# Kernel optimization log

Measured on AMD Instinct MI355X. Metric: run time of the kernel, lower is better.

The kernel has to match this reference:

```python
import jax, jax.numpy as jnp
import numpy as np

N_NODES = 100000
N_EDGES = 1600000
IN_DIM = 128
OUT_DIM = 128


def setup_inputs() -> dict:
    key = jax.random.key(0)
    ks = jax.random.split(key, 8)
    x = jax.random.normal(ks[0], (N_NODES, IN_DIM), dtype=jnp.float32)
    one_hot_h = jax.random.normal(ks[1], (N_NODES, OUT_DIM), dtype=jnp.float32)
    # three candidate-op linear transforms (in_dim -> out_dim)
    W0 = jax.random.normal(ks[2], (IN_DIM, OUT_DIM), dtype=jnp.float32) * 0.05
    W1 = jax.random.normal(ks[3], (IN_DIM, OUT_DIM), dtype=jnp.float32) * 0.05
    W2 = jax.random.normal(ks[4], (IN_DIM, OUT_DIM), dtype=jnp.float32) * 0.05
    # sparse mask_matrix in COO form: out[r] += v * H[c]
    mask_rows = jax.random.randint(ks[5], (N_EDGES,), 0, N_NODES, dtype=jnp.int32)
    mask_cols = jax.random.randint(ks[6], (N_EDGES,), 0, N_NODES, dtype=jnp.int32)
    mask_vals = jax.random.uniform(ks[7], (N_EDGES,), dtype=jnp.float32)
    return {"x": x, "one_hot_h": one_hot_h, "W0": W0, "W1": W1, "W2": W2,
            "mask_rows": mask_rows, "mask_cols": mask_cols, "mask_vals": mask_vals}


def reference(x, one_hot_h, W0, W1, W2, mask_rows, mask_cols, mask_vals):
    # Original: sum_k spmm(mask_matrix, op_k(x)) + spmm(mask_matrix, one_hot_h).
    # spmm is linear, so summing per-op outputs pre-aggregation is exact and
    # fuses K spmm launches into one sparse aggregation pass.
    H = x @ W0 + x @ W1 + x @ W2 + one_hot_h              # [N, out_dim]
    gathered = mask_vals[:, None] * H[mask_cols]          # [E, out_dim]
    out = jax.ops.segment_sum(gathered, mask_rows, num_segments=x.shape[0])
    return out
```

## Files before the change

### kernel.cpp

```cpp
#include <hip/hip_runtime.h>
#include <hip/hip_bf16.h>

#define N_NODES 100000
#define N_EDGES 1600000
#define DIM 128

#define NBIN 512
#define RPP  196
#define PCAP 4096
#define P1_BLOCKS 512
#define CHUNK (N_EDGES / P1_BLOCKS)

typedef unsigned int uint_t;
typedef unsigned short ushort_t;
typedef float f32x4 __attribute__((ext_vector_type(4)));
typedef __bf16 bf16x8 __attribute__((ext_vector_type(8)));

__device__ inline uint_t f2bf(float f) {
    uint_t u = __float_as_uint(f);
    return (u + 0x7FFFu + ((u >> 16) & 1u)) >> 16;
}
__device__ inline float bf2f(uint_t lo16) { return __uint_as_float(lo16 << 16); }

__global__ __launch_bounds__(256) void pass1_bin(
        const int* __restrict__ rows, const int* __restrict__ cols,
        const float* __restrict__ vals, int* __restrict__ psize,
        long long* __restrict__ slab,
        const float* __restrict__ W0, const float* __restrict__ W1,
        const float* __restrict__ W2, ushort_t* __restrict__ WT) {
    if (blockIdx.x >= P1_BLOCKS) {
        int i = (blockIdx.x - P1_BLOCKS) * 256 + threadIdx.x;
        if (i < DIM * DIM) {
            int m = i & 127, k = i >> 7;
            float s = W0[k * DIM + m] + W1[k * DIM + m] + W2[k * DIM + m];
            WT[m * DIM + k] = (ushort_t)f2bf(s);
        }
        return;
    }
    __shared__ int hist[NBIN];
    __shared__ int binoff[NBIN];
    __shared__ int resv[NBIN];
    __shared__ int curs[NBIN];
    __shared__ long long ebuf[CHUNK];
    __shared__ int edest[CHUNK];

    int t = threadIdx.x;
    int e0 = blockIdx.x * CHUNK;

    for (int i = t; i < NBIN; i += 256) hist[i] = 0;
    __syncthreads();

    for (int i = t; i < CHUNK; i += 256) {
        int r = rows[e0 + i];
        atomicAdd(&hist[r / RPP], 1);
    }
    __syncthreads();

    if (t < 64) {
        int b = t * 8;
        int v[8]; int s = 0;
#pragma unroll
        for (int k = 0; k < 8; ++k) { v[k] = hist[b + k]; s += v[k]; }
        int incl = s;
#pragma unroll
        for (int d = 1; d < 64; d <<= 1) {
            int o = __shfl_up(incl, d, 64);
            if (t >= d) incl += o;
        }
        int run = incl - s;
#pragma unroll
        for (int k = 0; k < 8; ++k) { binoff[b + k] = run; run += v[k]; }
    }
    __syncthreads();

    for (int i = t; i < NBIN; i += 256) {
        int len = hist[i];
        int r = (len > 0) ? atomicAdd(&psize[i], len) : 0;
        resv[i] = i * PCAP + r;
        curs[i] = binoff[i];
    }
    __syncthreads();

    for (int i = t; i < CHUNK; i += 256) {
        int   r = rows[e0 + i];
        int   c = cols[e0 + i];
        float v = vals[e0 + i];
        int b  = r / RPP;
        int lr = r - b * RPP;
        int pos = atomicAdd(&curs[b], 1);
        uint_t key = ((uint_t)lr << 17) | (uint_t)c;
        ebuf[pos]  = ((long long)__float_as_int(v) << 32) | (long long)key;
        edest[pos] = resv[b] + (pos - binoff[b]);
    }
    __syncthreads();

    for (int i = t; i < CHUNK; i += 256)
        slab[edest[i]] = ebuf[i];
}

__global__ __launch_bounds__(256) void pass2_sort(
        const long long* __restrict__ slab, const int* __restrict__ psize,
        int* __restrict__ off, long long* __restrict__ csr) {
    __shared__ int pb[NBIN + 1];
    __shared__ int cnt[RPP + 1];
    __shared__ int loff[RPP + 1];
    __shared__ int curs[RPP];
    __shared__ long long ebuf[PCAP];

    int p = blockIdx.x, t = threadIdx.x;

    if (t < 64) {
        int b = t * 8;
        int v[8]; int s = 0;
#pragma unroll
        for (int k = 0; k < 8; ++k) { v[k] = min(psize[b + k], PCAP); s += v[k]; }
        int incl = s;
#pragma unroll
        for (int d = 1; d < 64; d <<= 1) {
            int o = __shfl_up(incl, d, 64);
            if (t >= d) incl += o;
        }
        int run = incl - s;
#pragma unroll
        for (int k = 0; k < 8; ++k) { pb[b + k] = run; run += v[k]; }
        if (t == 63) pb[NBIN] = incl;
    }
    for (int i = t; i < RPP + 1; i += 256) cnt[i] = 0;
    __syncthreads();

    int n = min(psize[p], PCAP);
    int base = pb[p];
    int rlo = p * RPP;
    int nrows = N_NODES - rlo;
    if (nrows > RPP) nrows = RPP;
    if (nrows < 0) nrows = 0;
    const long long* seg = slab + (long long)p * PCAP;

    if (p == NBIN - 1 && t == 0) off[N_NODES] = pb[NBIN];

    for (int i = t; i < n; i += 256) {
        long long ev = __builtin_nontemporal_load(&seg[i]);
        ebuf[i] = ev;
        uint_t key = (uint_t)(ev & 0xFFFFFFFFll);
        atomicAdd(&cnt[key >> 17], 1);
    }
    __syncthreads();

    if (t < 64) {
        int b4 = t * 4;
        int v[4]; int s = 0;
#pragma unroll
        for (int k = 0; k < 4; ++k) {
            int idx = b4 + k;
            v[k] = (idx < RPP) ? cnt[idx] : 0;
            s += v[k];
        }
        int incl = s;
#pragma unroll
        for (int d = 1; d < 64; d <<= 1) {
            int o = __shfl_up(incl, d, 64);
            if (t >= d) incl += o;
        }
        int run = incl - s;
#pragma unroll
        for (int k = 0; k < 4; ++k) {
            int idx = b4 + k;
            if (idx < RPP) loff[idx] = run;
            run += v[k];
        }
    }
    __syncthreads();

    for (int i = t; i < nrows; i += 256) {
        curs[i] = loff[i];
        off[rlo + i] = base + loff[i];
    }
    __syncthreads();

    for (int i = t; i < n; i += 256) {
        long long ev = ebuf[i];
        uint_t key = (uint_t)(ev & 0xFFFFFFFFll);
        int lr = key >> 17;
        uint_t c = key & 0x1FFFFu;
        int pos = atomicAdd(&curs[lr], 1);
        csr[base + pos] = (long long)(((unsigned long long)ev & 0xFFFFFFFF00000000ull) | c);
    }
}

#define GROWS 64
#define XSTR 136
__global__ __launch_bounds__(256) void gemm_mfma(const float* __restrict__ x,
                                                 const float* __restrict__ oh,
                                                 const ushort_t* __restrict__ WT,
                                                 uint_t* __restrict__ H16) {
    __shared__ ushort_t xs[GROWS * XSTR];
    int tid = threadIdx.x;
    int wv = tid >> 6, l = tid & 63;
    int lr = l & 15, kg = l >> 4;
    int lrow = wv * 16 + lr;
    long long base_row = (long long)blockIdx.x * GROWS;
    long long hr = base_row + lrow;

    const f32x4* xg = (const f32x4*)x;
#pragma unroll
    for (int i = 0; i < 8; ++i) {
        int g = tid + i * 256;
        int row = g >> 5, c4 = g & 31;
        long long sr = base_row + row; if (sr >= N_NODES) sr = N_NODES - 1;
        f32x4 v = __builtin_nontemporal_load(xg + sr * 32 + c4);
        ushort_t* d = &xs[row * XSTR + c4 * 4];
        d[0] = (ushort_t)f2bf(v.x); d[1] = (ushort_t)f2bf(v.y);
        d[2] = (ushort_t)f2bf(v.z); d[3] = (ushort_t)f2bf(v.w);
    }
    __syncthreads();

    f32x4 acc[8] = {};
#pragma unroll
    for (int s = 0; s < 4; ++s) {
        bf16x8 b = *(const bf16x8*)&xs[lrow * XSTR + s * 32 + kg * 8];
#pragma unroll
        for (int mt = 0; mt < 8; ++mt) {
            bf16x8 a = *(const bf16x8*)&WT[(mt * 16 + lr) * DIM + s * 32 + kg * 8];
            acc[mt] = __builtin_amdgcn_mfma_f32_16x16x32_bf16(a, b, acc[mt], 0, 0, 0);
        }
    }
    __syncthreads();

    const f32x4* og = (const f32x4*)oh;
#pragma unroll
    for (int i = 0; i < 8; ++i) {
        int g = tid + i * 256;
        int row = g >> 5, c4 = g & 31;
        long long sr = base_row + row; if (sr >= N_NODES) sr = N_NODES - 1;
        f32x4 v = __builtin_nontemporal_load(og + sr * 32 + c4);
        ushort_t* d = &xs[row * XSTR + c4 * 4];
        d[0] = (ushort_t)f2bf(v.x); d[1] = (ushort_t)f2bf(v.y);
        d[2] = (ushort_t)f2bf(v.z); d[3] = (ushort_t)f2bf(v.w);
    }
    __syncthreads();

    if (hr < N_NODES) {
#pragma unroll
        for (int mt = 0; mt < 8; ++mt) {
            int c0 = mt * 16 + kg * 4;
            const uint_t* ow = (const uint_t*)&xs[lrow * XSTR + c0];
            uint_t w0 = ow[0], w1 = ow[1];
            float f0 = acc[mt].x + bf2f(w0 & 0xFFFFu);
            float f1 = acc[mt].y + bf2f(w0 >> 16);
            float f2 = acc[mt].z + bf2f(w1 & 0xFFFFu);
            float f3 = acc[mt].w + bf2f(w1 >> 16);
            uint2 pk;
            pk.x = f2bf(f0) | (f2bf(f1) << 16);
            pk.y = f2bf(f2) | (f2bf(f3) << 16);
            *(uint2*)&H16[(size_t)hr * (DIM / 2) + c0 / 2] = pk;
        }
    }
}

__global__ __launch_bounds__(256) void gather_kernel(const uint_t* __restrict__ H16,
                                                     const int* __restrict__ off,
                                                     const long long* __restrict__ csr,
                                                     float* __restrict__ out) {
    int tid  = threadIdx.x;
    int wave = tid >> 6;
    int lane = tid & 63;
    int grp  = lane >> 4;
    int il   = lane & 15;
    int wid  = blockIdx.x * 16 + wave * 4 + grp;

    int s = off[wid], e = off[wid + 1];
    float acc[8] = {};

#define ACC8(h, v)                                                            \
    acc[0] += (v) * bf2f((h).x & 0xFFFFu); acc[1] += (v) * bf2f((h).x >> 16); \
    acc[2] += (v) * bf2f((h).y & 0xFFFFu); acc[3] += (v) * bf2f((h).y >> 16); \
    acc[4] += (v) * bf2f((h).z & 0xFFFFu); acc[5] += (v) * bf2f((h).z >> 16); \
    acc[6] += (v) * bf2f((h).w & 0xFFFFu); acc[7] += (v) * bf2f((h).w >> 16);

    int p = s;
    for (; p + 3 < e; p += 4) {
        long long cv0 = __builtin_nontemporal_load(&csr[p]);
        long long cv1 = __builtin_nontemporal_load(&csr[p + 1]);
        long long cv2 = __builtin_nontemporal_load(&csr[p + 2]);
        long long cv3 = __builtin_nontemporal_load(&csr[p + 3]);
        uint4 h0 = *(const uint4*)&H16[(long long)(int)(cv0 & 0x1FFFF) * (DIM / 2) + il * 4];
        uint4 h1 = *(const uint4*)&H16[(long long)(int)(cv1 & 0x1FFFF) * (DIM / 2) + il * 4];
        uint4 h2 = *(const uint4*)&H16[(long long)(int)(cv2 & 0x1FFFF) * (DIM / 2) + il * 4];
        uint4 h3 = *(const uint4*)&H16[(long long)(int)(cv3 & 0x1FFFF) * (DIM / 2) + il * 4];
        float v0 = __int_as_float((int)(cv0 >> 32));
        float v1 = __int_as_float((int)(cv1 >> 32));
        float v2 = __int_as_float((int)(cv2 >> 32));
        float v3 = __int_as_float((int)(cv3 >> 32));
        ACC8(h0, v0) ACC8(h1, v1) ACC8(h2, v2) ACC8(h3, v3)
    }
    for (; p < e; ++p) {
        long long cv = __builtin_nontemporal_load(&csr[p]);
        float v = __int_as_float((int)(cv >> 32));
        uint4 h = *(const uint4*)&H16[(long long)(int)(cv & 0x1FFFF) * (DIM / 2) + il * 4];
        ACC8(h, v)
    }
#undef ACC8

    float* op = &out[(long long)wid * DIM + il * 8];
    f32x4 o0 = {acc[0], acc[1], acc[2], acc[3]};
    f32x4 o1 = {acc[4], acc[5], acc[6], acc[7]};
    __builtin_nontemporal_store(o0, (f32x4*)op);
    __builtin_nontemporal_store(o1, (f32x4*)(op + 4));
}

extern "C" void kernel_launch(void* const* d_in, const int* in_sizes, int n_in,
                              void* d_out, int out_size, void* d_ws, size_t ws_size,
                              hipStream_t stream) {
    const float* x    = (const float*)d_in[0];
    const float* oh   = (const float*)d_in[1];
    const float* W0   = (const float*)d_in[2];
    const float* W1   = (const float*)d_in[3];
    const float* W2   = (const float*)d_in[4];
    const int*   rows = (const int*)d_in[5];
    const int*   cols = (const int*)d_in[6];
    const float* vals = (const float*)d_in[7];
    float* out = (float*)d_out;

    char* p = (char*)d_ws;
    size_t oW    = 0;
    size_t oH    = oW + 64 * 1024;
    size_t oOff  = oH + (size_t)N_NODES * DIM * 2;
    size_t oPs   = oOff + (size_t)(N_NODES + 32) * 4;
    size_t oSlab = oPs + 4096;
    size_t oCsr  = oSlab + (size_t)NBIN * PCAP * 8;

    ushort_t*  WT    = (ushort_t*)(p + oW);
    uint_t*    H16   = (uint_t*)(p + oH);
    int*       off   = (int*)(p + oOff);
    int*       psize = (int*)(p + oPs);
    long long* slab  = (long long*)(p + oSlab);
    long long* csr   = (long long*)(p + oCsr);

    (void)hipMemsetAsync(psize, 0, NBIN * sizeof(int), stream);
    pass1_bin<<<P1_BLOCKS + 64, 256, 0, stream>>>(rows, cols, vals, psize, slab,
                                                  W0, W1, W2, WT);
    pass2_sort<<<NBIN, 256, 0, stream>>>(slab, psize, off, csr);
    gemm_mfma<<<(N_NODES + GROWS - 1) / GROWS, 256, 0, stream>>>(x, oh, WT, H16);
    gather_kernel<<<N_NODES / 16, 256, 0, stream>>>(H16, off, csr, out);
}
```

Before: 161.9 us.

## Fuse edge binning pass with dense GEMM into one interleaved launch

```diff
diff --git a/kernel.cpp b/kernel.cpp
--- a/kernel.cpp
+++ b/kernel.cpp
@@ -10,6 +10,7 @@
 #define PCAP 4096
 #define P1_BLOCKS 512
 #define CHUNK (N_EDGES / P1_BLOCKS)
+#define GEMM_BLOCKS 1563
 
 typedef unsigned int uint_t;
 typedef unsigned short ushort_t;
@@ -22,80 +23,166 @@
 }
 __device__ inline float bf2f(uint_t lo16) { return __uint_as_float(lo16 << 16); }
 
-__global__ __launch_bounds__(256) void pass1_bin(
+__global__ __launch_bounds__(256) void wt_init(const float* __restrict__ W0,
+                                               const float* __restrict__ W1,
+                                               const float* __restrict__ W2,
+                                               ushort_t* __restrict__ WT,
+                                               int* __restrict__ psize) {
+    if (blockIdx.x == 64) {
+        int i = threadIdx.x;
+        if (i < NBIN / 2) { ((int2*)psize)[i] = make_int2(0, 0); }
+        return;
+    }
+    int i = blockIdx.x * 256 + threadIdx.x;
+    int m = i & 127, k = i >> 7;
+    float s = W0[k * DIM + m] + W1[k * DIM + m] + W2[k * DIM + m];
+    WT[m * DIM + k] = (ushort_t)f2bf(s);
+}
+
+#define GROWS 64
+#define XSTR 136
+
+__global__ __launch_bounds__(256) void fused_p1_gemm(
         const int* __restrict__ rows, const int* __restrict__ cols,
         const float* __restrict__ vals, int* __restrict__ psize,
         long long* __restrict__ slab,
-        const float* __restrict__ W0, const float* __restrict__ W1,
-        const float* __restrict__ W2, ushort_t* __restrict__ WT) {
-    if (blockIdx.x >= P1_BLOCKS) {
-        int i = (blockIdx.x - P1_BLOCKS) * 256 + threadIdx.x;
-        if (i < DIM * DIM) {
-            int m = i & 127, k = i >> 7;
-            float s = W0[k * DIM + m] + W1[k * DIM + m] + W2[k * DIM + m];
-            WT[m * DIM + k] = (ushort_t)f2bf(s);
-        }
-        return;
-    }
-    __shared__ int hist[NBIN];
-    __shared__ int binoff[NBIN];
-    __shared__ int resv[NBIN];
-    __shared__ int curs[NBIN];
-    __shared__ long long ebuf[CHUNK];
-    __shared__ int edest[CHUNK];
-
+        const float* __restrict__ x, const float* __restrict__ oh,
+        const ushort_t* __restrict__ WT, uint_t* __restrict__ H16) {
+    __shared__ __align__(16) char smem[8192 + CHUNK * 8 + CHUNK * 4];
+
+    int role, idx;
+    if (blockIdx.x < 2048) {
+        int g = blockIdx.x >> 2, sb = blockIdx.x & 3;
+        if (sb == 3) { role = 1; idx = g; }
+        else         { role = 0; idx = g * 3 + sb; }
+    } else {
+        role = 0; idx = 1536 + (int)(blockIdx.x - 2048);
+    }
     int t = threadIdx.x;
-    int e0 = blockIdx.x * CHUNK;
-
-    for (int i = t; i < NBIN; i += 256) hist[i] = 0;
-    __syncthreads();
-
-    for (int i = t; i < CHUNK; i += 256) {
-        int r = rows[e0 + i];
-        atomicAdd(&hist[r / RPP], 1);
-    }
-    __syncthreads();
-
-    if (t < 64) {
-        int b = t * 8;
-        int v[8]; int s = 0;
-#pragma unroll
-        for (int k = 0; k < 8; ++k) { v[k] = hist[b + k]; s += v[k]; }
-        int incl = s;
-#pragma unroll
-        for (int d = 1; d < 64; d <<= 1) {
-            int o = __shfl_up(incl, d, 64);
-            if (t >= d) incl += o;
-        }
-        int run = incl - s;
-#pragma unroll
-        for (int k = 0; k < 8; ++k) { binoff[b + k] = run; run += v[k]; }
-    }
-    __syncthreads();
-
-    for (int i = t; i < NBIN; i += 256) {
-        int len = hist[i];
-        int r = (len > 0) ? atomicAdd(&psize[i], len) : 0;
-        resv[i] = i * PCAP + r;
-        curs[i] = binoff[i];
-    }
-    __syncthreads();
-
-    for (int i = t; i < CHUNK; i += 256) {
-        int   r = rows[e0 + i];
-        int   c = cols[e0 + i];
-        float v = vals[e0 + i];
-        int b  = r / RPP;
-        int lr = r - b * RPP;
-        int pos = atomicAdd(&curs[b], 1);
-        uint_t key = ((uint_t)lr << 17) | (uint_t)c;
-        ebuf[pos]  = ((long long)__float_as_int(v) << 32) | (long long)key;
-        edest[pos] = resv[b] + (pos - binoff[b]);
-    }
-    __syncthreads();
-
-    for (int i = t; i < CHUNK; i += 256)
-        slab[edest[i]] = ebuf[i];
+
+    if (role == 1) {
+        int* hist   = (int*)smem;
+        int* binoff = hist + NBIN;
+        int* resv   = binoff + NBIN;
+        int* curs   = resv + NBIN;
+        long long* ebuf = (long long*)(smem + 8192);
+        int* edest  = (int*)(smem + 8192 + CHUNK * 8);
+
+        int e0 = idx * CHUNK;
+
+        for (int i = t; i < NBIN; i += 256) hist[i] = 0;
+        __syncthreads();
+
+        for (int i = t; i < CHUNK; i += 256) {
+            int r = rows[e0 + i];
+            atomicAdd(&hist[r / RPP], 1);
+        }
+        __syncthreads();
+
+        if (t < 64) {
+            int b = t * 8;
+            int v[8]; int s = 0;
+#pragma unroll
+            for (int k = 0; k < 8; ++k) { v[k] = hist[b + k]; s += v[k]; }
+            int incl = s;
+#pragma unroll
+            for (int d = 1; d < 64; d <<= 1) {
+                int o = __shfl_up(incl, d, 64);
+                if (t >= d) incl += o;
+            }
+            int run = incl - s;
+#pragma unroll
+            for (int k = 0; k < 8; ++k) { binoff[b + k] = run; run += v[k]; }
+        }
+        __syncthreads();
+
+        for (int i = t; i < NBIN; i += 256) {
+            int len = hist[i];
+            int r = (len > 0) ? atomicAdd(&psize[i], len) : 0;
+            resv[i] = i * PCAP + r;
+            curs[i] = binoff[i];
+        }
+        __syncthreads();
+
+        for (int i = t; i < CHUNK; i += 256) {
+            int   r = rows[e0 + i];
+            int   c = cols[e0 + i];
+            float v = vals[e0 + i];
+            int b  = r / RPP;
+            int lr = r - b * RPP;
+            int pos = atomicAdd(&curs[b], 1);
+            uint_t key = ((uint_t)lr << 17) | (uint_t)c;
+            ebuf[pos]  = ((long long)__float_as_int(v) << 32) | (long long)key;
+            edest[pos] = resv[b] + (pos - binoff[b]);
+        }
+        __syncthreads();
+
+        for (int i = t; i < CHUNK; i += 256)
+            slab[edest[i]] = ebuf[i];
+    } else {
+        ushort_t* xs = (ushort_t*)smem;
+
+        int wv = t >> 6, l = t & 63;
+        int lr = l & 15, kg = l >> 4;
+        int lrow = wv * 16 + lr;
+        long long base_row = (long long)idx * GROWS;
+        long long hr = base_row + lrow;
+
+        const f32x4* xg = (const f32x4*)x;
+#pragma unroll
+        for (int i = 0; i < 8; ++i) {
+            int g = t + i * 256;
+            int row = g >> 5, c4 = g & 31;
+            long long sr = base_row + row; if (sr >= N_NODES) sr = N_NODES - 1;
+            f32x4 v = __builtin_nontemporal_load(xg + sr * 32 + c4);
+            ushort_t* d = &xs[row * XSTR + c4 * 4];
+            d[0] = (ushort_t)f2bf(v.x); d[1] = (ushort_t)f2bf(v.y);
+            d[2] = (ushort_t)f2bf(v.z); d[3] = (ushort_t)f2bf(v.w);
+        }
+        __syncthreads();
+
+        f32x4 acc[8] = {};
+#pragma unroll
+        for (int s = 0; s < 4; ++s) {
+            bf16x8 b = *(const bf16x8*)&xs[lrow * XSTR + s * 32 + kg * 8];
+#pragma unroll
+            for (int mt = 0; mt < 8; ++mt) {
+                bf16x8 a = *(const bf16x8*)&WT[(mt * 16 + lr) * DIM + s * 32 + kg * 8];
+                acc[mt] = __builtin_amdgcn_mfma_f32_16x16x32_bf16(a, b, acc[mt], 0, 0, 0);
+            }
+        }
+        __syncthreads();
+
+        const f32x4* og = (const f32x4*)oh;
+#pragma unroll
+        for (int i = 0; i < 8; ++i) {
+            int g = t + i * 256;
+            int row = g >> 5, c4 = g & 31;
+            long long sr = base_row + row; if (sr >= N_NODES) sr = N_NODES - 1;
+            f32x4 v = __builtin_nontemporal_load(og + sr * 32 + c4);
+            ushort_t* d = &xs[row * XSTR + c4 * 4];
+            d[0] = (ushort_t)f2bf(v.x); d[1] = (ushort_t)f2bf(v.y);
+            d[2] = (ushort_t)f2bf(v.z); d[3] = (ushort_t)f2bf(v.w);
+        }
+        __syncthreads();
+
+        if (hr < N_NODES) {
+#pragma unroll
+            for (int mt = 0; mt < 8; ++mt) {
+                int c0 = mt * 16 + kg * 4;
+                const uint_t* ow = (const uint_t*)&xs[lrow * XSTR + c0];
+                uint_t w0 = ow[0], w1 = ow[1];
+                float f0 = acc[mt].x + bf2f(w0 & 0xFFFFu);
+                float f1 = acc[mt].y + bf2f(w0 >> 16);
+                float f2 = acc[mt].z + bf2f(w1 & 0xFFFFu);
+                float f3 = acc[mt].w + bf2f(w1 >> 16);
+                uint2 pk;
+                pk.x = f2bf(f0) | (f2bf(f1) << 16);
+                pk.y = f2bf(f2) | (f2bf(f3) << 16);
+                *(uint2*)&H16[(size_t)hr * (DIM / 2) + c0 / 2] = pk;
+            }
+        }
+    }
 }
 
 __global__ __launch_bounds__(256) void pass2_sort(
@@ -184,76 +271,6 @@
         uint_t c = key & 0x1FFFFu;
         int pos = atomicAdd(&curs[lr], 1);
         csr[base + pos] = (long long)(((unsigned long long)ev & 0xFFFFFFFF00000000ull) | c);
-    }
-}
-
-#define GROWS 64
-#define XSTR 136
-__global__ __launch_bounds__(256) void gemm_mfma(const float* __restrict__ x,
-                                                 const float* __restrict__ oh,
-                                                 const ushort_t* __restrict__ WT,
-                                                 uint_t* __restrict__ H16) {
-    __shared__ ushort_t xs[GROWS * XSTR];
-    int tid = threadIdx.x;
-    int wv = tid >> 6, l = tid & 63;
-    int lr = l & 15, kg = l >> 4;
-    int lrow = wv * 16 + lr;
-    long long base_row = (long long)blockIdx.x * GROWS;
-    long long hr = base_row + lrow;
-
-    const f32x4* xg = (const f32x4*)x;
-#pragma unroll
-    for (int i = 0; i < 8; ++i) {
-        int g = tid + i * 256;
-        int row = g >> 5, c4 = g & 31;
-        long long sr = base_row + row; if (sr >= N_NODES) sr = N_NODES - 1;
-        f32x4 v = __builtin_nontemporal_load(xg + sr * 32 + c4);
-        ushort_t* d = &xs[row * XSTR + c4 * 4];
-        d[0] = (ushort_t)f2bf(v.x); d[1] = (ushort_t)f2bf(v.y);
-        d[2] = (ushort_t)f2bf(v.z); d[3] = (ushort_t)f2bf(v.w);
-    }
-    __syncthreads();
-
-    f32x4 acc[8] = {};
-#pragma unroll
-    for (int s = 0; s < 4; ++s) {
-        bf16x8 b = *(const bf16x8*)&xs[lrow * XSTR + s * 32 + kg * 8];
-#pragma unroll
-        for (int mt = 0; mt < 8; ++mt) {
-            bf16x8 a = *(const bf16x8*)&WT[(mt * 16 + lr) * DIM + s * 32 + kg * 8];
-            acc[mt] = __builtin_amdgcn_mfma_f32_16x16x32_bf16(a, b, acc[mt], 0, 0, 0);
-        }
-    }
-    __syncthreads();
-
-    const f32x4* og = (const f32x4*)oh;
-#pragma unroll
-    for (int i = 0; i < 8; ++i) {
-        int g = tid + i * 256;
-        int row = g >> 5, c4 = g & 31;
-        long long sr = base_row + row; if (sr >= N_NODES) sr = N_NODES - 1;
-        f32x4 v = __builtin_nontemporal_load(og + sr * 32 + c4);
-        ushort_t* d = &xs[row * XSTR + c4 * 4];
-        d[0] = (ushort_t)f2bf(v.x); d[1] = (ushort_t)f2bf(v.y);
-        d[2] = (ushort_t)f2bf(v.z); d[3] = (ushort_t)f2bf(v.w);
-    }
-    __syncthreads();
-
-    if (hr < N_NODES) {
-#pragma unroll
-        for (int mt = 0; mt < 8; ++mt) {
-            int c0 = mt * 16 + kg * 4;
-            const uint_t* ow = (const uint_t*)&xs[lrow * XSTR + c0];
-            uint_t w0 = ow[0], w1 = ow[1];
-            float f0 = acc[mt].x + bf2f(w0 & 0xFFFFu);
-            float f1 = acc[mt].y + bf2f(w0 >> 16);
-            float f2 = acc[mt].z + bf2f(w1 & 0xFFFFu);
-            float f3 = acc[mt].w + bf2f(w1 >> 16);
-            uint2 pk;
-            pk.x = f2bf(f0) | (f2bf(f1) << 16);
-            pk.y = f2bf(f2) | (f2bf(f3) << 16);
-            *(uint2*)&H16[(size_t)hr * (DIM / 2) + c0 / 2] = pk;
-        }
     }
 }
 
@@ -336,10 +353,9 @@
     long long* slab  = (long long*)(p + oSlab);
     long long* csr   = (long long*)(p + oCsr);
 
-    (void)hipMemsetAsync(psize, 0, NBIN * sizeof(int), stream);
-    pass1_bin<<<P1_BLOCKS + 64, 256, 0, stream>>>(rows, cols, vals, psize, slab,
-                                                  W0, W1, W2, WT);
+    wt_init<<<65, 256, 0, stream>>>(W0, W1, W2, WT, psize);
+    fused_p1_gemm<<<2075, 256, 0, stream>>>(rows, cols, vals, psize, slab,
+                                            x, oh, WT, H16);
     pass2_sort<<<NBIN, 256, 0, stream>>>(slab, psize, off, csr);
-    gemm_mfma<<<(N_NODES + GROWS - 1) / GROWS, 256, 0, stream>>>(x, oh, WT, H16);
     gather_kernel<<<N_NODES / 16, 256, 0, stream>>>(H16, off, csr, out);
 }
```

After: 151.3 us. 1.07x faster.

## Fuse per-bin CSR sort and MFMA GEMM into one heterogeneous launch

Applied to the files above, without the earlier changes.

```diff
diff --git a/kernel.cpp b/kernel.cpp
--- a/kernel.cpp
+++ b/kernel.cpp
@@ -22,7 +22,7 @@
 }
 __device__ inline float bf2f(uint_t lo16) { return __uint_as_float(lo16 << 16); }
 
-__global__ __launch_bounds__(256) void pass1_bin(
+__global__ __launch_bounds__(256) void pass1_wt(
         const int* __restrict__ rows, const int* __restrict__ cols,
         const float* __restrict__ vals, int* __restrict__ psize,
         long long* __restrict__ slab,
@@ -30,11 +30,9 @@
         const float* __restrict__ W2, ushort_t* __restrict__ WT) {
     if (blockIdx.x >= P1_BLOCKS) {
         int i = (blockIdx.x - P1_BLOCKS) * 256 + threadIdx.x;
-        if (i < DIM * DIM) {
-            int m = i & 127, k = i >> 7;
-            float s = W0[k * DIM + m] + W1[k * DIM + m] + W2[k * DIM + m];
-            WT[m * DIM + k] = (ushort_t)f2bf(s);
-        }
+        int m = i & 127, k = i >> 7;
+        float s = W0[k * DIM + m] + W1[k * DIM + m] + W2[k * DIM + m];
+        WT[m * DIM + k] = (ushort_t)f2bf(s);
         return;
     }
     __shared__ int hist[NBIN];
@@ -98,161 +96,175 @@
         slab[edest[i]] = ebuf[i];
 }
 
-__global__ __launch_bounds__(256) void pass2_sort(
-        const long long* __restrict__ slab, const int* __restrict__ psize,
-        int* __restrict__ off, long long* __restrict__ csr) {
-    __shared__ int pb[NBIN + 1];
-    __shared__ int cnt[RPP + 1];
-    __shared__ int loff[RPP + 1];
-    __shared__ int curs[RPP];
-    __shared__ long long ebuf[PCAP];
-
-    int p = blockIdx.x, t = threadIdx.x;
-
-    if (t < 64) {
-        int b = t * 8;
-        int v[8]; int s = 0;
-#pragma unroll
-        for (int k = 0; k < 8; ++k) { v[k] = min(psize[b + k], PCAP); s += v[k]; }
-        int incl = s;
-#pragma unroll
-        for (int d = 1; d < 64; d <<= 1) {
-            int o = __shfl_up(incl, d, 64);
-            if (t >= d) incl += o;
-        }
-        int run = incl - s;
-#pragma unroll
-        for (int k = 0; k < 8; ++k) { pb[b + k] = run; run += v[k]; }
-        if (t == 63) pb[NBIN] = incl;
-    }
-    for (int i = t; i < RPP + 1; i += 256) cnt[i] = 0;
-    __syncthreads();
-
-    int n = min(psize[p], PCAP);
-    int base = pb[p];
-    int rlo = p * RPP;
-    int nrows = N_NODES - rlo;
-    if (nrows > RPP) nrows = RPP;
-    if (nrows < 0) nrows = 0;
-    const long long* seg = slab + (long long)p * PCAP;
-
-    if (p == NBIN - 1 && t == 0) off[N_NODES] = pb[NBIN];
-
-    for (int i = t; i < n; i += 256) {
-        long long ev = __builtin_nontemporal_load(&seg[i]);
-        ebuf[i] = ev;
-        uint_t key = (uint_t)(ev & 0xFFFFFFFFll);
-        atomicAdd(&cnt[key >> 17], 1);
-    }
-    __syncthreads();
-
-    if (t < 64) {
-        int b4 = t * 4;
-        int v[4]; int s = 0;
-#pragma unroll
-        for (int k = 0; k < 4; ++k) {
-            int idx = b4 + k;
-            v[k] = (idx < RPP) ? cnt[idx] : 0;
-            s += v[k];
-        }
-        int incl = s;
-#pragma unroll
-        for (int d = 1; d < 64; d <<= 1) {
-            int o = __shfl_up(incl, d, 64);
-            if (t >= d) incl += o;
-        }
-        int run = incl - s;
-#pragma unroll
-        for (int k = 0; k < 4; ++k) {
-            int idx = b4 + k;
-            if (idx < RPP) loff[idx] = run;
-            run += v[k];
-        }
-    }
-    __syncthreads();
-
-    for (int i = t; i < nrows; i += 256) {
-        curs[i] = loff[i];
-        off[rlo + i] = base + loff[i];
-    }
-    __syncthreads();
-
-    for (int i = t; i < n; i += 256) {
-        long long ev = ebuf[i];
-        uint_t key = (uint_t)(ev & 0xFFFFFFFFll);
-        int lr = key >> 17;
-        uint_t c = key & 0x1FFFFu;
-        int pos = atomicAdd(&curs[lr], 1);
-        csr[base + pos] = (long long)(((unsigned long long)ev & 0xFFFFFFFF00000000ull) | c);
-    }
-}
-
 #define GROWS 64
 #define XSTR 136
-__global__ __launch_bounds__(256) void gemm_mfma(const float* __restrict__ x,
-                                                 const float* __restrict__ oh,
-                                                 const ushort_t* __restrict__ WT,
-                                                 uint_t* __restrict__ H16) {
-    __shared__ ushort_t xs[GROWS * XSTR];
-    int tid = threadIdx.x;
-    int wv = tid >> 6, l = tid & 63;
-    int lr = l & 15, kg = l >> 4;
-    int lrow = wv * 16 + lr;
-    long long base_row = (long long)blockIdx.x * GROWS;
-    long long hr = base_row + lrow;
-
-    const f32x4* xg = (const f32x4*)x;
-#pragma unroll
-    for (int i = 0; i < 8; ++i) {
-        int g = tid + i * 256;
-        int row = g >> 5, c4 = g & 31;
-        long long sr = base_row + row; if (sr >= N_NODES) sr = N_NODES - 1;
-        f32x4 v = __builtin_nontemporal_load(xg + sr * 32 + c4);
-        ushort_t* d = &xs[row * XSTR + c4 * 4];
-        d[0] = (ushort_t)f2bf(v.x); d[1] = (ushort_t)f2bf(v.y);
-        d[2] = (ushort_t)f2bf(v.z); d[3] = (ushort_t)f2bf(v.w);
-    }
-    __syncthreads();
-
-    f32x4 acc[8] = {};
-#pragma unroll
-    for (int s = 0; s < 4; ++s) {
-        bf16x8 b = *(const bf16x8*)&xs[lrow * XSTR + s * 32 + kg * 8];
-#pragma unroll
-        for (int mt = 0; mt < 8; ++mt) {
-            bf16x8 a = *(const bf16x8*)&WT[(mt * 16 + lr) * DIM + s * 32 + kg * 8];
-            acc[mt] = __builtin_amdgcn_mfma_f32_16x16x32_bf16(a, b, acc[mt], 0, 0, 0);
-        }
-    }
-    __syncthreads();
-
-    const f32x4* og = (const f32x4*)oh;
-#pragma unroll
-    for (int i = 0; i < 8; ++i) {
-        int g = tid + i * 256;
-        int row = g >> 5, c4 = g & 31;
-        long long sr = base_row + row; if (sr >= N_NODES) sr = N_NODES - 1;
-        f32x4 v = __builtin_nontemporal_load(og + sr * 32 + c4);
-        ushort_t* d = &xs[row * XSTR + c4 * 4];
-        d[0] = (ushort_t)f2bf(v.x); d[1] = (ushort_t)f2bf(v.y);
-        d[2] = (ushort_t)f2bf(v.z); d[3] = (ushort_t)f2bf(v.w);
-    }
-    __syncthreads();
-
-    if (hr < N_NODES) {
-#pragma unroll
-        for (int mt = 0; mt < 8; ++mt) {
-            int c0 = mt * 16 + kg * 4;
-            const uint_t* ow = (const uint_t*)&xs[lrow * XSTR + c0];
-            uint_t w0 = ow[0], w1 = ow[1];
-            float f0 = acc[mt].x + bf2f(w0 & 0xFFFFu);
-            float f1 = acc[mt].y + bf2f(w0 >> 16);
-            float f2 = acc[mt].z + bf2f(w1 & 0xFFFFu);
-            float f3 = acc[mt].w + bf2f(w1 >> 16);
-            uint2 pk;
-            pk.x = f2bf(f0) | (f2bf(f1) << 16);
-            pk.y = f2bf(f2) | (f2bf(f3) << 16);
-            *(uint2*)&H16[(size_t)hr * (DIM / 2) + c0 / 2] = pk;
+#define SM_INTS 4412
+#define SM_EBUF 4416
+
+__global__ __launch_bounds__(256) void fused_p2_gemm(
+        const long long* __restrict__ slab, const int* __restrict__ psize,
+        int* __restrict__ off, long long* __restrict__ csr,
+        const float* __restrict__ x, const float* __restrict__ oh,
+        const ushort_t* __restrict__ WT, uint_t* __restrict__ H16) {
+    __shared__ __align__(16) char smem[SM_EBUF + PCAP * 8];
+
+    int role, idx;
+    if (blockIdx.x < 2048) {
+        int g = blockIdx.x >> 2, sb = blockIdx.x & 3;
+        if (sb == 3) { role = 1; idx = g; }
+        else         { role = 0; idx = g * 3 + sb; }
+    } else {
+        role = 0; idx = 1536 + (int)(blockIdx.x - 2048);
+    }
+    int t = threadIdx.x;
+
+    if (role == 1) {
+        int* pb   = (int*)smem;
+        int* cnt  = pb + NBIN + 1;
+        int* loff = cnt + RPP + 1;
+        int* curs = loff + RPP + 1;
+        long long* ebuf = (long long*)(smem + SM_EBUF);
+
+        int p = idx;
+
+        if (t < 64) {
+            int b = t * 8;
+            int v[8]; int s = 0;
+#pragma unroll
+            for (int k = 0; k < 8; ++k) { v[k] = min(psize[b + k], PCAP); s += v[k]; }
+            int incl = s;
+#pragma unroll
+            for (int d = 1; d < 64; d <<= 1) {
+                int o = __shfl_up(incl, d, 64);
+                if (t >= d) incl += o;
+            }
+            int run = incl - s;
+#pragma unroll
+            for (int k = 0; k < 8; ++k) { pb[b + k] = run; run += v[k]; }
+            if (t == 63) pb[NBIN] = incl;
+        }
+        for (int i = t; i < RPP + 1; i += 256) cnt[i] = 0;
+        __syncthreads();
+
+        int n = min(psize[p], PCAP);
+        int base = pb[p];
+        int rlo = p * RPP;
+        int nrows = N_NODES - rlo;
+        if (nrows > RPP) nrows = RPP;
+        if (nrows < 0) nrows = 0;
+        const long long* seg = slab + (long long)p * PCAP;
+
+        if (p == NBIN - 1 && t == 0) off[N_NODES] = pb[NBIN];
+
+        for (int i = t; i < n; i += 256) {
+            long long ev = __builtin_nontemporal_load(&seg[i]);
+            ebuf[i] = ev;
+            uint_t key = (uint_t)(ev & 0xFFFFFFFFll);
+            atomicAdd(&cnt[key >> 17], 1);
+        }
+        __syncthreads();
+
+        if (t < 64) {
+            int b4 = t * 4;
+            int v[4]; int s = 0;
+#pragma unroll
+            for (int k = 0; k < 4; ++k) {
+                int idx2 = b4 + k;
+                v[k] = (idx2 < RPP) ? cnt[idx2] : 0;
+                s += v[k];
+            }
+            int incl = s;
+#pragma unroll
+            for (int d = 1; d < 64; d <<= 1) {
+                int o = __shfl_up(incl, d, 64);
+                if (t >= d) incl += o;
+            }
+            int run = incl - s;
+#pragma unroll
+            for (int k = 0; k < 4; ++k) {
+                int idx2 = b4 + k;
+                if (idx2 < RPP) loff[idx2] = run;
+                run += v[k];
+            }
+        }
+        __syncthreads();
+
+        for (int i = t; i < nrows; i += 256) {
+            curs[i] = loff[i];
+            off[rlo + i] = base + loff[i];
+        }
+        __syncthreads();
+
+        for (int i = t; i < n; i += 256) {
+            long long ev = ebuf[i];
+            uint_t key = (uint_t)(ev & 0xFFFFFFFFll);
+            int lr = key >> 17;
+            uint_t c = key & 0x1FFFFu;
+            int pos = atomicAdd(&curs[lr], 1);
+            csr[base + pos] = (long long)(((unsigned long long)ev & 0xFFFFFFFF00000000ull) | c);
+        }
+    } else {
+        ushort_t* xs = (ushort_t*)smem;
+
+        int wv = t >> 6, l = t & 63;
+        int lr = l & 15, kg = l >> 4;
+        int lrow = wv * 16 + lr;
+        long long base_row = (long long)idx * GROWS;
+        long long hr = base_row + lrow;
+
+        const f32x4* xg = (const f32x4*)x;
+#pragma unroll
+        for (int i = 0; i < 8; ++i) {
+            int g = t + i * 256;
+            int row = g >> 5, c4 = g & 31;
+            long long sr = base_row + row; if (sr >= N_NODES) sr = N_NODES - 1;
+            f32x4 v = __builtin_nontemporal_load(xg + sr * 32 + c4);
+            ushort_t* d = &xs[row * XSTR + c4 * 4];
+            d[0] = (ushort_t)f2bf(v.x); d[1] = (ushort_t)f2bf(v.y);
+            d[2] = (ushort_t)f2bf(v.z); d[3] = (ushort_t)f2bf(v.w);
+        }
+        __syncthreads();
+
+        f32x4 acc[8] = {};
+#pragma unroll
+        for (int s = 0; s < 4; ++s) {
+            bf16x8 b = *(const bf16x8*)&xs[lrow * XSTR + s * 32 + kg * 8];
+#pragma unroll
+            for (int mt = 0; mt < 8; ++mt) {
+                bf16x8 a = *(const bf16x8*)&WT[(mt * 16 + lr) * DIM + s * 32 + kg * 8];
+                acc[mt] = __builtin_amdgcn_mfma_f32_16x16x32_bf16(a, b, acc[mt], 0, 0, 0);
+            }
+        }
+        __syncthreads();
+
+        const f32x4* og = (const f32x4*)oh;
+#pragma unroll
+        for (int i = 0; i < 8; ++i) {
+            int g = t + i * 256;
+            int row = g >> 5, c4 = g & 31;
+            long long sr = base_row + row; if (sr >= N_NODES) sr = N_NODES - 1;
+            f32x4 v = __builtin_nontemporal_load(og + sr * 32 + c4);
+            ushort_t* d = &xs[row * XSTR + c4 * 4];
+            d[0] = (ushort_t)f2bf(v.x); d[1] = (ushort_t)f2bf(v.y);
+            d[2] = (ushort_t)f2bf(v.z); d[3] = (ushort_t)f2bf(v.w);
+        }
+        __syncthreads();
+
+        if (hr < N_NODES) {
+#pragma unroll
+            for (int mt = 0; mt < 8; ++mt) {
+                int c0 = mt * 16 + kg * 4;
+                const uint_t* ow = (const uint_t*)&xs[lrow * XSTR + c0];
+                uint_t w0 = ow[0], w1 = ow[1];
+                float f0 = acc[mt].x + bf2f(w0 & 0xFFFFu);
+                float f1 = acc[mt].y + bf2f(w0 >> 16);
+                float f2 = acc[mt].z + bf2f(w1 & 0xFFFFu);
+                float f3 = acc[mt].w + bf2f(w1 >> 16);
+                uint2 pk;
+                pk.x = f2bf(f0) | (f2bf(f1) << 16);
+                pk.y = f2bf(f2) | (f2bf(f3) << 16);
+                *(uint2*)&H16[(size_t)hr * (DIM / 2) + c0 / 2] = pk;
+            }
         }
     }
 }
@@ -337,9 +349,8 @@
     long long* csr   = (long long*)(p + oCsr);
 
     (void)hipMemsetAsync(psize, 0, NBIN * sizeof(int), stream);
-    pass1_bin<<<P1_BLOCKS + 64, 256, 0, stream>>>(rows, cols, vals, psize, slab,
-                                                  W0, W1, W2, WT);
-    pass2_sort<<<NBIN, 256, 0, stream>>>(slab, psize, off, csr);
-    gemm_mfma<<<(N_NODES + GROWS - 1) / GROWS, 256, 0, stream>>>(x, oh, WT, H16);
+    pass1_wt<<<P1_BLOCKS + 64, 256, 0, stream>>>(rows, cols, vals, psize, slab,
+                                                 W0, W1, W2, WT);
+    fused_p2_gemm<<<2075, 256, 0, stream>>>(slab, psize, off, csr, x, oh, WT, H16);
     gather_kernel<<<N_NODES / 16, 256, 0, stream>>>(H16, off, csr, out);
 }
```

Result: faster. 158.6 us (-2.0%).
